# Performance work log

Hardware: AMD Instinct MI355X
Metric: run time of the kernel (lower is better)

Reference implementation:

```python
import jax, jax.numpy as jnp
import numpy as np

B, D, H = 64, 2048, 2048


def setup_inputs() -> dict:
    key = jax.random.key(0)
    ks = jax.random.split(key, 10)
    s = 1.0 / np.sqrt(D)  # Linear init scale
    # small z scale keeps exp() gates in a sane range
    return {
        "t": jnp.zeros((), jnp.float32),
        "z": jax.random.normal(ks[0], (B, D), jnp.float32) * 0.02,
        "K": jax.random.normal(ks[1], (B, D), jnp.float32) * 0.02,
        "V": jax.random.normal(ks[2], (B, D, D), jnp.float32) * 0.02,
        "Wq": jax.random.normal(ks[3], (D, D), jnp.float32) * s,
        "bq": jnp.zeros((D,), jnp.float32),
        "Wk": jax.random.normal(ks[4], (D, D), jnp.float32) * s,
        "bk": jnp.zeros((D,), jnp.float32),
        "Wv": jax.random.normal(ks[5], (D, D), jnp.float32) * s,
        "bv": jnp.zeros((D,), jnp.float32),
        "W1": jax.random.normal(ks[6], (D, H), jnp.float32) * s,
        "b1": jnp.zeros((H,), jnp.float32),
        "W2": jax.random.normal(ks[7], (H, D), jnp.float32) * (1.0 / np.sqrt(H)),
        "b2": jnp.zeros((D,), jnp.float32),
    }


def reference(t, z, K, V, Wq, bq, Wk, bk, Wv, bv, W1, b1, W2, b2):
    # get_ode_gradient_nn: 2-layer tanh MLP (stand-in for user ode_func_net)
    dz = jnp.tanh(z @ W1 + b1) @ W2 + b2                 # [B, D]
    dK = jnp.exp(z @ Wk + bk)                            # exp gate, [B, D]
    v = z @ Wv + bv                                      # [B, D]
    dV = jnp.einsum("bd,be->bde", v, dK)                # rank-1 outer update, [B, D, D]
    q = jnp.exp(z @ Wq + bq)                             # [B, D]
    a = jnp.sum(q * dK, axis=-1, keepdims=True)          # q . dK, [B, 1]
    dq = q * (dz @ Wq + bq)                              # [B, D]
    da = a + jnp.sum(dq * K, axis=-1, keepdims=True)     # [B, 1]
    dc = jnp.einsum("bde,be->bd", dV, q) + jnp.einsum("bde,be->bd", V, dq)  # [B, D]
    return (dz, da, dc, dK, dV)
```

## Files before the change

kernel.cpp:

```cpp
#include <hip/hip_runtime.h>
#include <cstddef>
#include <math.h>

#define BB 64
#define DD 2048
#define HH 2048
#define BD (BB*DD)
#define WN (2048*2048)

typedef unsigned short u16;
typedef __attribute__((ext_vector_type(8))) short bf16x8;
typedef __attribute__((ext_vector_type(4))) float f32x4;
typedef __attribute__((ext_vector_type(4))) float f4;

__device__ __forceinline__ u16 f2b(float x) {
    union { float f; unsigned u; } v; v.f = x;
    unsigned r = v.u + 0x7FFFu + ((v.u >> 16) & 1u);
    return (u16)(r >> 16);
}

__device__ __forceinline__ void gload16(const void* g, void* l) {
    __builtin_amdgcn_global_load_lds(
        (__attribute__((address_space(1))) void*)g,
        (__attribute__((address_space(3))) void*)l, 16, 0, 0);
}


__device__ __forceinline__ void wconv_tile(
    u16* sm, const float* __restrict__ W, u16* __restrict__ T,
    int kb, int nb)
{
    int t = threadIdx.x;
    int k0 = kb * 64, n0 = nb * 64;
    {
        int r = t >> 2, c0 = (t & 3) * 16;
        const float* src = W + (size_t)(k0 + r) * DD + n0 + c0;
#pragma unroll
        for (int q = 0; q < 4; ++q) {
            float4 f = *(const float4*)(src + q * 4);
            sm[r * 66 + c0 + q*4 + 0] = f2b(f.x);
            sm[r * 66 + c0 + q*4 + 1] = f2b(f.y);
            sm[r * 66 + c0 + q*4 + 2] = f2b(f.z);
            sm[r * 66 + c0 + q*4 + 3] = f2b(f.w);
        }
    }
    __syncthreads();
    {
        int rn = t >> 2, ck = (t & 3) * 16;
        u16 o[16];
#pragma unroll
        for (int j = 0; j < 16; ++j) o[j] = sm[(ck + j) * 66 + rn];
        u16* dst = T + (size_t)(n0 + rn) * DD + k0 + ck;
        *(bf16x8*)dst       = *(bf16x8*)&o[0];
        *(bf16x8*)(dst + 8) = *(bf16x8*)&o[8];
    }
}

template<int NS>
__device__ __forceinline__ void gemm_fullk(
    u16* sm, const u16* __restrict__ A0, const u16* __restrict__ A1,
    const u16* __restrict__ Wt, int nblk, f32x4* acc0, f32x4* acc1)
{
    constexpr int NS1 = NS + 1;
    constexpr int REG = NS1 * 2048;
    const int t = threadIdx.x, w = t >> 6, lane = t & 63;
    const int n0 = nblk * 64;
    const int srow = lane >> 2;
    const int sk   = (lane & 3) * 8;

    const u16* gA0 = A0 + (size_t)(w * 16 + srow) * DD + sk;
    const u16* gA1 = (NS == 2) ? A1 + (size_t)(w * 16 + srow) * DD + sk : A0;
    const u16* gW  = Wt + (size_t)(n0 + w * 16 + srow) * DD + sk;
    const int woff = w * 512;

    const int lane15 = lane & 15;
    const int k8 = (lane >> 4) * 8;

    auto stage = [&](int it, int buf) {
        u16* base = sm + buf * REG;
        gload16(gA0 + it * 32, base + woff);
        if constexpr (NS == 2) gload16(gA1 + it * 32, base + 2048 + woff);
        gload16(gW + it * 32, base + (NS1 - 1) * 2048 + woff);
    };

    constexpr int nt = DD / 32;
    stage(0, 0);
    stage(1, 1);
    for (int it = 0; it < nt; ++it) {
        const int cur = it % 3;
        if (it + 2 < nt) {
            stage(it + 2, (it + 2) % 3);
            if constexpr (NS == 1) asm volatile("s_waitcnt vmcnt(4)" ::: "memory");
            else                   asm volatile("s_waitcnt vmcnt(6)" ::: "memory");
        } else if (it + 1 < nt) {
            if constexpr (NS == 1) asm volatile("s_waitcnt vmcnt(2)" ::: "memory");
            else                   asm volatile("s_waitcnt vmcnt(3)" ::: "memory");
        } else {
            asm volatile("s_waitcnt vmcnt(0)" ::: "memory");
        }
        __builtin_amdgcn_s_barrier();

        const u16* base = sm + cur * REG;
        bf16x8 bfrag = *(const bf16x8*)&base[(NS1-1)*2048 + (w*16 + lane15)*32 + k8];
#pragma unroll
        for (int mt = 0; mt < 4; ++mt) {
            bf16x8 a0 = *(const bf16x8*)&base[(mt*16 + lane15)*32 + k8];
            acc0[mt] = __builtin_amdgcn_mfma_f32_16x16x32_bf16(a0, bfrag, acc0[mt], 0, 0, 0);
        }
        if constexpr (NS == 2) {
#pragma unroll
            for (int mt = 0; mt < 4; ++mt) {
                bf16x8 a1 = *(const bf16x8*)&base[2048 + (mt*16 + lane15)*32 + k8];
                acc1[mt] = __builtin_amdgcn_mfma_f32_16x16x32_bf16(a1, bfrag, acc1[mt], 0, 0, 0);
            }
        }
        __builtin_amdgcn_s_barrier();
    }
}

__device__ __forceinline__ void dv_body(
    const float* __restrict__ v, const float* __restrict__ dK,
    float* __restrict__ dV, int b, int chunk)
{
    int wave = threadIdx.x >> 6;
    int lane = threadIdx.x & 63;

    const f4* dK4 = (const f4*)(dK + ((size_t)b << 11));
    f4 dKr[8];
#pragma unroll
    for (int u = 0; u < 8; ++u) dKr[u] = dK4[u * 64 + lane];

    int row0 = chunk * 64 + wave * 16;
    for (int rr = 0; rr < 16; ++rr) {
        int row = row0 + rr;
        float vr = v[((size_t)b << 11) + row];
        f4* dV4 = (f4*)(dV + (((size_t)((b << 11) | row)) << 11));
#pragma unroll
        for (int u = 0; u < 8; ++u) {
            f4 o = vr * dKr[u];
            __builtin_nontemporal_store(o, &dV4[u * 64 + lane]);
        }
    }
}


__global__ __launch_bounds__(256) void wconv1(
    const float* __restrict__ W1, const float* __restrict__ Wk,
    const float* __restrict__ Wv, u16* __restrict__ W1t,
    u16* __restrict__ Wkt, u16* __restrict__ Wvt,
    const float* __restrict__ z, u16* __restrict__ zb)
{
    __shared__ u16 sm[64 * 66];
    int t = threadIdx.x;
    if (blockIdx.z == 3) {
        if (blockIdx.y != 0 || blockIdx.x >= 32) return;
        int i0 = blockIdx.x * 4096 + t * 16;
        u16 o[16];
#pragma unroll
        for (int q = 0; q < 4; ++q) {
            float4 f = *(const float4*)&z[i0 + q * 4];
            o[q*4+0] = f2b(f.x); o[q*4+1] = f2b(f.y);
            o[q*4+2] = f2b(f.z); o[q*4+3] = f2b(f.w);
        }
        *(bf16x8*)&zb[i0]     = *(bf16x8*)&o[0];
        *(bf16x8*)&zb[i0 + 8] = *(bf16x8*)&o[8];
        return;
    }
    const float* W = (blockIdx.z == 0) ? W1 : (blockIdx.z == 1) ? Wk : Wv;
    u16* T = (blockIdx.z == 0) ? W1t : (blockIdx.z == 1) ? Wkt : Wvt;
    wconv_tile(sm, W, T, blockIdx.x, blockIdx.y);
}

__global__ __launch_bounds__(256) void mA(
    const u16* __restrict__ zb, const u16* __restrict__ W1t,
    const u16* __restrict__ Wkt, const u16* __restrict__ Wvt,
    const float* __restrict__ b1, const float* __restrict__ bk,
    const float* __restrict__ bv, u16* __restrict__ hb,
    float* __restrict__ dKo, float* __restrict__ vo,
    const float* __restrict__ W2, const float* __restrict__ Wq,
    u16* __restrict__ W2t, u16* __restrict__ Wqt)
{
    __shared__ u16 sm[3 * 4096];
    int blk = blockIdx.x;
    if (blk < 96) {
        int sel  = blk >> 5;
        int nblk = blk & 31;
        const u16* Wt = (sel == 0) ? W1t : (sel == 1) ? Wkt : Wvt;
        f32x4 acc[4];
#pragma unroll
        for (int mt = 0; mt < 4; ++mt) acc[mt] = (f32x4){0.f,0.f,0.f,0.f};
        gemm_fullk<1>(sm, zb, zb, Wt, nblk, acc, nullptr);

        int w = threadIdx.x >> 6, lane = threadIdx.x & 63;
        int col = nblk * 64 + w * 16 + (lane & 15);
        int r4  = (lane >> 4) * 4;
        if (sel == 0) {
            float bb = b1[col];
#pragma unroll
            for (int mt = 0; mt < 4; ++mt)
#pragma unroll
                for (int j = 0; j < 4; ++j)
                    hb[(size_t)(mt*16 + r4 + j) * DD + col] =
                        f2b(tanhf(acc[mt][j] + bb));
        } else if (sel == 1) {
            float bb = bk[col];
#pragma unroll
            for (int mt = 0; mt < 4; ++mt)
#pragma unroll
                for (int j = 0; j < 4; ++j)
                    dKo[(size_t)(mt*16 + r4 + j) * DD + col] =
                        expf(acc[mt][j] + bb);
        } else {
            float bb = bv[col];
#pragma unroll
            for (int mt = 0; mt < 4; ++mt)
#pragma unroll
                for (int j = 0; j < 4; ++j)
                    vo[(size_t)(mt*16 + r4 + j) * DD + col] =
                        acc[mt][j] + bb;
        }
    } else {
        int r = blk - 96;
        const float* W = (r < 1024) ? W2 : Wq;
        u16* T         = (r < 1024) ? W2t : Wqt;
        int rr = r & 1023;
        wconv_tile(sm, W, T, rr & 31, rr >> 5);
    }
}

__global__ __launch_bounds__(256) void mDZ(
    const u16* __restrict__ hb, const u16* __restrict__ W2t,
    const float* __restrict__ b2, float* __restrict__ dz,
    u16* __restrict__ dzb,
    const float* __restrict__ v, const float* __restrict__ dK,
    float* __restrict__ dV)
{
    __shared__ u16 sm[3 * 4096];
    int blk = blockIdx.x;
    if (blk < 32) {
        f32x4 acc[4];
#pragma unroll
        for (int mt = 0; mt < 4; ++mt) acc[mt] = (f32x4){0.f,0.f,0.f,0.f};
        gemm_fullk<1>(sm, hb, hb, W2t, blk, acc, nullptr);

        int w = threadIdx.x >> 6, lane = threadIdx.x & 63;
        int col = blk * 64 + w * 16 + (lane & 15);
        int r4  = (lane >> 4) * 4;
        float bb = b2[col];
#pragma unroll
        for (int mt = 0; mt < 4; ++mt)
#pragma unroll
            for (int j = 0; j < 4; ++j) {
                float s = acc[mt][j] + bb;
                size_t idx = (size_t)(mt*16 + r4 + j) * DD + col;
                dz[idx]  = s;
                dzb[idx] = f2b(s);
            }
    } else {
        int r = blk - 32;
        dv_body(v, dK, dV, r >> 5, r & 31);
    }
}

__global__ __launch_bounds__(256) void mQ(
    const u16* __restrict__ zb, const u16* __restrict__ dzb,
    const u16* __restrict__ Wqt, const float* __restrict__ bq,
    float* __restrict__ qo, float* __restrict__ dqo,
    const float* __restrict__ v, const float* __restrict__ dK,
    float* __restrict__ dV)
{
    __shared__ u16 sm[3 * 6144];
    int blk = blockIdx.x;
    if (blk < 32) {
        f32x4 az[4], ad[4];
#pragma unroll
        for (int mt = 0; mt < 4; ++mt) {
            az[mt] = (f32x4){0.f,0.f,0.f,0.f};
            ad[mt] = (f32x4){0.f,0.f,0.f,0.f};
        }
        gemm_fullk<2>(sm, zb, dzb, Wqt, blk, az, ad);

        int w = threadIdx.x >> 6, lane = threadIdx.x & 63;
        int col = blk * 64 + w * 16 + (lane & 15);
        int r4  = (lane >> 4) * 4;
        float bb = bq[col];
#pragma unroll
        for (int mt = 0; mt < 4; ++mt)
#pragma unroll
            for (int j = 0; j < 4; ++j) {
                float qv = expf(az[mt][j] + bb);
                size_t idx = (size_t)(mt*16 + r4 + j) * DD + col;
                qo[idx]  = qv;
                dqo[idx] = qv * (ad[mt][j] + bb);
            }
    } else {
        int r = blk - 32;
        dv_body(v, dK, dV, 32 + (r >> 5), r & 31);
    }
}

__global__ __launch_bounds__(256) void reduce_a_da(
    const float* __restrict__ q, const float* __restrict__ dK,
    const float* __restrict__ dq, const float* __restrict__ Kin,
    float* __restrict__ a_ws, float* __restrict__ da_out)
{
    int b = blockIdx.x;
    int t = threadIdx.x;
    const float* qb  = q   + (size_t)b * DD;
    const float* dKb = dK  + (size_t)b * DD;
    const float* dqb = dq  + (size_t)b * DD;
    const float* Kb  = Kin + (size_t)b * DD;

    float s1 = 0.f, s2 = 0.f;
    for (int i = t; i < DD; i += 256) {
        s1 = fmaf(qb[i],  dKb[i], s1);
        s2 = fmaf(dqb[i], Kb[i],  s2);
    }
#pragma unroll
    for (int off = 32; off; off >>= 1) {
        s1 += __shfl_down(s1, off);
        s2 += __shfl_down(s2, off);
    }
    __shared__ float r1[4], r2[4];
    if ((t & 63) == 0) { r1[t >> 6] = s1; r2[t >> 6] = s2; }
    __syncthreads();
    if (t == 0) {
        float a  = r1[0] + r1[1] + r1[2] + r1[3];
        float k2 = r2[0] + r2[1] + r2[2] + r2[3];
        a_ws[b]   = a;
        da_out[b] = a + k2;
    }
}

__global__ __launch_bounds__(256) void dc_dot(
    const float* __restrict__ V, const float* __restrict__ v,
    const float* __restrict__ dq, const float* __restrict__ a,
    float* __restrict__ dc)
{
    int b     = blockIdx.x >> 5;
    int chunk = blockIdx.x & 31;
    int wave  = threadIdx.x >> 6;
    int lane  = threadIdx.x & 63;

    const f4* dq4 = (const f4*)(dq + ((size_t)b << 11));
    f4 dqr[8];
#pragma unroll
    for (int u = 0; u < 8; ++u) dqr[u] = dq4[u * 64 + lane];
    float ab = a[b];

    int row0 = chunk * 64 + wave * 16;
    for (int g = 0; g < 4; ++g) {
        float dot[4];
#pragma unroll
        for (int r2i = 0; r2i < 4; ++r2i) {
            int row = row0 + g * 4 + r2i;
            const f4* V4 = (const f4*)(V + (((size_t)((b << 11) | row)) << 11));
            float d = 0.f;
#pragma unroll
            for (int u = 0; u < 8; ++u) {
                f4 Vv = __builtin_nontemporal_load(&V4[u * 64 + lane]);
                d += Vv[0] * dqr[u][0] + Vv[1] * dqr[u][1]
                   + Vv[2] * dqr[u][2] + Vv[3] * dqr[u][3];
            }
            dot[r2i] = d;
        }
#pragma unroll
        for (int r2i = 0; r2i < 4; ++r2i) {
            float d = dot[r2i];
#pragma unroll
            for (int s = 32; s; s >>= 1) d += __shfl_down(d, s);
            if (lane == 0) {
                int row = row0 + g * 4 + r2i;
                dc[((size_t)b << 11) + row] =
                    v[((size_t)b << 11) + row] * ab + d;
            }
        }
    }
}

template<int MT>
__device__ __forceinline__ void gemm_body_f32(
    const float* __restrict__ A0, const float* __restrict__ A1,
    const float* __restrict__ W, float* __restrict__ part, int kc)
{
    constexpr int KC = 32;
    constexpr int RT = MT / 16;
    __shared__ float As[KC][MT];
    __shared__ float Ws[KC][64];

    const int t  = threadIdx.x;
    const int n0 = blockIdx.x * 64;
    const int k0 = blockIdx.y * kc;
    const int i  = t >> 4;
    const int j  = t & 15;

    float acc[RT][4];
#pragma unroll
    for (int r = 0; r < RT; ++r)
#pragma unroll
        for (int c = 0; c < 4; ++c) acc[r][c] = 0.f;

    for (int kk0 = 0; kk0 < kc; kk0 += KC) {
        {
            int kk = t >> 3;
            int nn = (t & 7) << 3;
            const float* s = W + (size_t)(k0 + kk0 + kk) * DD + n0 + nn;
            *(float4*)&Ws[kk][nn]     = *(const float4*)s;
            *(float4*)&Ws[kk][nn + 4] = *(const float4*)(s + 4);
        }
        if constexpr (MT == 64) {
            int m  = t & 63;
            int kb = (t >> 6) << 3;
            const float* s = A0 + (size_t)m * DD + k0 + kk0 + kb;
            float4 a0 = *(const float4*)s;
            float4 a1 = *(const float4*)(s + 4);
            As[kb+0][m] = a0.x; As[kb+1][m] = a0.y;
            As[kb+2][m] = a0.z; As[kb+3][m] = a0.w;
            As[kb+4][m] = a1.x; As[kb+5][m] = a1.y;
            As[kb+6][m] = a1.z; As[kb+7][m] = a1.w;
        } else {
            int m  = t & 127;
            int kb = (t >> 7) << 4;
            const float* base = (m < 64) ? (A0 + (size_t)m * DD)
                                         : (A1 + (size_t)(m - 64) * DD);
            const float* s = base + k0 + kk0 + kb;
#pragma unroll
            for (int p = 0; p < 4; ++p) {
                float4 av = *(const float4*)(s + p * 4);
                As[kb+p*4+0][m] = av.x; As[kb+p*4+1][m] = av.y;
                As[kb+p*4+2][m] = av.z; As[kb+p*4+3][m] = av.w;
            }
        }
        __syncthreads();
#pragma unroll
        for (int kk = 0; kk < KC; ++kk) {
            float4 wv = *(float4*)&Ws[kk][j << 2];
#pragma unroll
            for (int rq = 0; rq < RT / 4; ++rq) {
                float4 av = *(float4*)&As[kk][i * RT + rq * 4];
                acc[rq*4+0][0] = fmaf(av.x, wv.x, acc[rq*4+0][0]);
                acc[rq*4+0][1] = fmaf(av.x, wv.y, acc[rq*4+0][1]);
                acc[rq*4+0][2] = fmaf(av.x, wv.z, acc[rq*4+0][2]);
                acc[rq*4+0][3] = fmaf(av.x, wv.w, acc[rq*4+0][3]);
                acc[rq*4+1][0] = fmaf(av.y, wv.x, acc[rq*4+1][0]);
                acc[rq*4+1][1] = fmaf(av.y, wv.y, acc[rq*4+1][1]);
                acc[rq*4+1][2] = fmaf(av.y, wv.z, acc[rq*4+1][2]);
                acc[rq*4+1][3] = fmaf(av.y, wv.w, acc[rq*4+1][3]);
                acc[rq*4+2][0] = fmaf(av.z, wv.x, acc[rq*4+2][0]);
                acc[rq*4+2][1] = fmaf(av.z, wv.y, acc[rq*4+2][1]);
                acc[rq*4+2][2] = fmaf(av.z, wv.z, acc[rq*4+2][2]);
                acc[rq*4+2][3] = fmaf(av.z, wv.w, acc[rq*4+2][3]);
                acc[rq*4+3][0] = fmaf(av.w, wv.x, acc[rq*4+3][0]);
                acc[rq*4+3][1] = fmaf(av.w, wv.y, acc[rq*4+3][1]);
                acc[rq*4+3][2] = fmaf(av.w, wv.z, acc[rq*4+3][2]);
                acc[rq*4+3][3] = fmaf(av.w, wv.w, acc[rq*4+3][3]);
            }
        }
        __syncthreads();
    }

    float* P = part + (size_t)blockIdx.y * MT * DD + n0 + (j << 2);
#pragma unroll
    for (int r = 0; r < RT; ++r)
        *(float4*)&P[(size_t)(i * RT + r) * DD] =
            make_float4(acc[r][0], acc[r][1], acc[r][2], acc[r][3]);
}

__global__ __launch_bounds__(256) void gemm64(
    const float* __restrict__ A, const float* __restrict__ W,
    float* __restrict__ part, int kc)
{ gemm_body_f32<64>(A, A, W, part, kc); }

__global__ __launch_bounds__(256) void gemm64_z2(
    const float* __restrict__ A,
    const float* __restrict__ W0, const float* __restrict__ W1,
    float* __restrict__ p0, float* __restrict__ p1, int kc)
{
    const float* W = blockIdx.z ? W1 : W0;
    float*       P = blockIdx.z ? p1 : p0;
    gemm_body_f32<64>(A, A, W, P, kc);
}

__global__ __launch_bounds__(256) void gemm128(
    const float* __restrict__ A0, const float* __restrict__ A1,
    const float* __restrict__ W, float* __restrict__ part, int kc)
{ gemm_body_f32<128>(A0, A1, W, part, kc); }

__global__ __launch_bounds__(256) void epilogue_f32(
    const float* __restrict__ part, const float* __restrict__ bias,
    float* __restrict__ out, int act, int KS)
{
    int i = blockIdx.x * 256 + threadIdx.x;
    float s = bias[i & (DD - 1)];
    for (int ks = 0; ks < KS; ++ks) s += part[(size_t)ks * BD + i];
    if (act == 1) s = tanhf(s);
    out[i] = s;
}

__global__ __launch_bounds__(256) void ep_kv_f32(
    const float* __restrict__ pk, const float* __restrict__ pv,
    const float* __restrict__ bk, const float* __restrict__ bv,
    float* __restrict__ dKo, float* __restrict__ vo, int KS)
{
    int i = blockIdx.x * 256 + threadIdx.x;
    int d = i & (DD - 1);
    float sk = 0.f, sv = 0.f;
    for (int ks = 0; ks < KS; ++ks) {
        sk += pk[(size_t)ks * BD + i];
        sv += pv[(size_t)ks * BD + i];
    }
    dKo[i] = expf(sk + bk[d]);
    vo[i]  = sv + bv[d];
}

__global__ __launch_bounds__(256) void ep_q_dq_f32(
    const float* __restrict__ pq, const float* __restrict__ bq,
    float* __restrict__ qo, float* __restrict__ dqo, int KS)
{
    int i = blockIdx.x * 256 + threadIdx.x;
    int b = i >> 11, d = i & (DD - 1);
    float sq = 0.f, sd = 0.f;
    for (int ks = 0; ks < KS; ++ks) {
        const float* P = pq + (size_t)ks * (128 * DD);
        sq += P[(size_t)b * DD + d];
        sd += P[(size_t)(b + 64) * DD + d];
    }
    float bb = bq[d];
    float qv = expf(sq + bb);
    qo[i]  = qv;
    dqo[i] = qv * (sd + bb);
}

__global__ __launch_bounds__(256) void dv_write_full(
    const float* __restrict__ v, const float* __restrict__ dK,
    float* __restrict__ dV)
{
    dv_body(v, dK, dV, blockIdx.x >> 5, blockIdx.x & 31);
}

extern "C" void kernel_launch(void* const* d_in, const int* in_sizes, int n_in,
                              void* d_out, int out_size, void* d_ws, size_t ws_size,
                              hipStream_t stream)
{
    const float* z   = (const float*)d_in[1];
    const float* Kin = (const float*)d_in[2];
    const float* Vin = (const float*)d_in[3];
    const float* Wq  = (const float*)d_in[4];
    const float* bq  = (const float*)d_in[5];
    const float* Wk  = (const float*)d_in[6];
    const float* bk  = (const float*)d_in[7];
    const float* Wv  = (const float*)d_in[8];
    const float* bv  = (const float*)d_in[9];
    const float* W1  = (const float*)d_in[10];
    const float* b1  = (const float*)d_in[11];
    const float* W2  = (const float*)d_in[12];
    const float* b2  = (const float*)d_in[13];

    float* out   = (float*)d_out;
    float* o_dz  = out;
    float* o_da  = out + BD;
    float* o_dc  = out + BD + BB;
    float* o_dK  = out + 2 * BD + BB;
    float* o_dV  = out + 3 * BD + BB;

    float* ws    = (float*)d_ws;
    float* ws_v  = ws;
    float* ws_q  = ws + BD;
    float* ws_dq = ws + 2 * BD;
    float* ws_a  = ws + 3 * BD;
    float* ws_h  = ws + 3 * BD + 64;
    u16*   zb    = (u16*)(ws + 4 * BD + 64);
    u16*   hb    = zb + BD;
    u16*   dzb   = hb + BD;
    u16*   wt    = dzb + BD;

    const size_t pre_fl = 4ull * BD + 64 + (3ull * BD + 5ull * WN) / 2;

    dim3 blk(256);

    if (pre_fl * 4ull <= ws_size) {
        u16* W1t = wt;
        u16* W2t = wt + 1ull * WN;
        u16* Wkt = wt + 2ull * WN;
        u16* Wvt = wt + 3ull * WN;
        u16* Wqt = wt + 4ull * WN;

        wconv1<<<dim3(32, 32, 4), blk, 0, stream>>>(
            W1, Wk, Wv, W1t, Wkt, Wvt, z, zb);

        mA<<<dim3(96 + 2048), blk, 0, stream>>>(
            zb, W1t, Wkt, Wvt, b1, bk, bv, hb, o_dK, ws_v, W2, Wq, W2t, Wqt);

        mDZ<<<dim3(32 + 1024), blk, 0, stream>>>(
            hb, W2t, b2, o_dz, dzb, ws_v, o_dK, o_dV);

        mQ<<<dim3(32 + 1024), blk, 0, stream>>>(
            zb, dzb, Wqt, bq, ws_q, ws_dq, ws_v, o_dK, o_dV);
    } else {
        float* pool = ws + 4 * BD + 64;
        int KSf = 16;
        while (KSf > 1 &&
               ((size_t)(4 * BD + 64) + 2ull * KSf * BD) * 4ull > ws_size)
            KSf >>= 1;
        int kc = DD / KSf;
        float* p0 = pool;
        float* p1 = pool + (size_t)KSf * BD;

        dim3 gG(DD / 64, KSf);
        dim3 gG2(DD / 64, KSf, 2);
        dim3 gE(BD / 256);

        gemm64<<<gG, blk, 0, stream>>>(z, W1, p0, kc);
        epilogue_f32<<<gE, blk, 0, stream>>>(p0, b1, ws_h, 1, KSf);

        gemm64<<<gG, blk, 0, stream>>>(ws_h, W2, p0, kc);
        epilogue_f32<<<gE, blk, 0, stream>>>(p0, b2, o_dz, 0, KSf);

        gemm64_z2<<<gG2, blk, 0, stream>>>(z, Wk, Wv, p0, p1, kc);
        ep_kv_f32<<<gE, blk, 0, stream>>>(p0, p1, bk, bv, o_dK, ws_v, KSf);

        dv_write_full<<<dim3(BB * 32), blk, 0, stream>>>(ws_v, o_dK, o_dV);

        gemm128<<<gG, blk, 0, stream>>>(z, o_dz, Wq, p0, kc);
        ep_q_dq_f32<<<gE, blk, 0, stream>>>(p0, bq, ws_q, ws_dq, KSf);
    }

    reduce_a_da<<<dim3(BB), blk, 0, stream>>>(ws_q, o_dK, ws_dq, Kin, ws_a, o_da);

    dc_dot<<<dim3(BB * 32), blk, 0, stream>>>(Vin, ws_v, ws_dq, ws_a, o_dc);
}
```

Baseline: 411.5 us.

## Fuse fp32 weight conversion into GEMM staging, dropping pre-transposed bf16 weight copies

```diff
diff --git a/kernel.cpp b/kernel.cpp
--- a/kernel.cpp
+++ b/kernel.cpp
@@ -6,7 +6,6 @@
 #define DD 2048
 #define HH 2048
 #define BD (BB*DD)
-#define WN (2048*2048)
 
 typedef unsigned short u16;
 typedef __attribute__((ext_vector_type(8))) short bf16x8;
@@ -19,102 +18,89 @@
     return (u16)(r >> 16);
 }
 
-__device__ __forceinline__ void gload16(const void* g, void* l) {
-    __builtin_amdgcn_global_load_lds(
-        (__attribute__((address_space(1))) void*)g,
-        (__attribute__((address_space(3))) void*)l, 16, 0, 0);
-}
-
-
-__device__ __forceinline__ void wconv_tile(
-    u16* sm, const float* __restrict__ W, u16* __restrict__ T,
-    int kb, int nb)
-{
-    int t = threadIdx.x;
-    int k0 = kb * 64, n0 = nb * 64;
-    {
-        int r = t >> 2, c0 = (t & 3) * 16;
-        const float* src = W + (size_t)(k0 + r) * DD + n0 + c0;
-#pragma unroll
-        for (int q = 0; q < 4; ++q) {
-            float4 f = *(const float4*)(src + q * 4);
-            sm[r * 66 + c0 + q*4 + 0] = f2b(f.x);
-            sm[r * 66 + c0 + q*4 + 1] = f2b(f.y);
-            sm[r * 66 + c0 + q*4 + 2] = f2b(f.z);
-            sm[r * 66 + c0 + q*4 + 3] = f2b(f.w);
-        }
-    }
-    __syncthreads();
-    {
-        int rn = t >> 2, ck = (t & 3) * 16;
-        u16 o[16];
-#pragma unroll
-        for (int j = 0; j < 16; ++j) o[j] = sm[(ck + j) * 66 + rn];
-        u16* dst = T + (size_t)(n0 + rn) * DD + k0 + ck;
-        *(bf16x8*)dst       = *(bf16x8*)&o[0];
-        *(bf16x8*)(dst + 8) = *(bf16x8*)&o[8];
-    }
-}
-
 template<int NS>
-__device__ __forceinline__ void gemm_fullk(
+__device__ __forceinline__ void gemm_fk2(
     u16* sm, const u16* __restrict__ A0, const u16* __restrict__ A1,
-    const u16* __restrict__ Wt, int nblk, f32x4* acc0, f32x4* acc1)
+    const float* __restrict__ W, int nblk, f32x4* acc0, f32x4* acc1)
 {
     constexpr int NS1 = NS + 1;
     constexpr int REG = NS1 * 2048;
     const int t = threadIdx.x, w = t >> 6, lane = t & 63;
     const int n0 = nblk * 64;
-    const int srow = lane >> 2;
-    const int sk   = (lane & 3) * 8;
-
-    const u16* gA0 = A0 + (size_t)(w * 16 + srow) * DD + sk;
-    const u16* gA1 = (NS == 2) ? A1 + (size_t)(w * 16 + srow) * DD + sk : A0;
-    const u16* gW  = Wt + (size_t)(n0 + w * 16 + srow) * DD + sk;
-    const int woff = w * 512;
-
+
+    const int am  = t >> 2;
+    const int ak8 = (t & 3) * 8;
+    const int kp = t >> 4;
+    const int c4 = (t & 15) * 4;
     const int lane15 = lane & 15;
-    const int k8 = (lane >> 4) * 8;
-
-    auto stage = [&](int it, int buf) {
-        u16* base = sm + buf * REG;
-        gload16(gA0 + it * 32, base + woff);
-        if constexpr (NS == 2) gload16(gA1 + it * 32, base + 2048 + woff);
-        gload16(gW + it * 32, base + (NS1 - 1) * 2048 + woff);
+    const int k8f = (lane >> 4) * 8;
+
+    const u16* pa0 = A0 + (size_t)am * DD + ak8;
+    const u16* pa1 = (NS == 2) ? A1 + (size_t)am * DD + ak8 : pa0;
+    const float* pw = W + (size_t)(2 * kp) * DD + n0 + c4;
+
+    struct R { bf16x8 a0; bf16x8 a1; float4 w0, w1; };
+    R Ra, Rb;
+
+    auto issue = [&](int it, R& r) {
+        r.a0 = *(const bf16x8*)(pa0 + it * 32);
+        if constexpr (NS == 2) r.a1 = *(const bf16x8*)(pa1 + it * 32);
+        r.w0 = *(const float4*)(pw + (size_t)it * 32 * DD);
+        r.w1 = *(const float4*)(pw + (size_t)it * 32 * DD + DD);
     };
-
-    constexpr int nt = DD / 32;
-    stage(0, 0);
-    stage(1, 1);
-    for (int it = 0; it < nt; ++it) {
-        const int cur = it % 3;
-        if (it + 2 < nt) {
-            stage(it + 2, (it + 2) % 3);
-            if constexpr (NS == 1) asm volatile("s_waitcnt vmcnt(4)" ::: "memory");
-            else                   asm volatile("s_waitcnt vmcnt(6)" ::: "memory");
-        } else if (it + 1 < nt) {
-            if constexpr (NS == 1) asm volatile("s_waitcnt vmcnt(2)" ::: "memory");
-            else                   asm volatile("s_waitcnt vmcnt(3)" ::: "memory");
-        } else {
-            asm volatile("s_waitcnt vmcnt(0)" ::: "memory");
-        }
+    auto store = [&](R& r, u16* buf) {
+        *(bf16x8*)(buf + am * 32 + ak8) = r.a0;
+        if constexpr (NS == 2)
+            *(bf16x8*)(buf + 2048 + am * 32 + ak8) = r.a1;
+        u16* wb = buf + (NS1 - 1) * 2048;
+        unsigned p;
+        p = (unsigned)f2b(r.w0.x) | ((unsigned)f2b(r.w1.x) << 16);
+        *(unsigned*)(wb + (c4 + 0) * 32 + 2 * kp) = p;
+        p = (unsigned)f2b(r.w0.y) | ((unsigned)f2b(r.w1.y) << 16);
+        *(unsigned*)(wb + (c4 + 1) * 32 + 2 * kp) = p;
+        p = (unsigned)f2b(r.w0.z) | ((unsigned)f2b(r.w1.z) << 16);
+        *(unsigned*)(wb + (c4 + 2) * 32 + 2 * kp) = p;
+        p = (unsigned)f2b(r.w0.w) | ((unsigned)f2b(r.w1.w) << 16);
+        *(unsigned*)(wb + (c4 + 3) * 32 + 2 * kp) = p;
+    };
+    auto compute = [&](const u16* buf) {
+        bf16x8 bfrag = *(const bf16x8*)(buf + (NS1 - 1) * 2048
+                                        + (w * 16 + lane15) * 32 + k8f);
+#pragma unroll
+        for (int mt = 0; mt < 4; ++mt) {
+            bf16x8 a = *(const bf16x8*)(buf + (mt * 16 + lane15) * 32 + k8f);
+            acc0[mt] = __builtin_amdgcn_mfma_f32_16x16x32_bf16(
+                a, bfrag, acc0[mt], 0, 0, 0);
+        }
+        if constexpr (NS == 2) {
+#pragma unroll
+            for (int mt = 0; mt < 4; ++mt) {
+                bf16x8 a = *(const bf16x8*)(buf + 2048
+                                            + (mt * 16 + lane15) * 32 + k8f);
+                acc1[mt] = __builtin_amdgcn_mfma_f32_16x16x32_bf16(
+                    a, bfrag, acc1[mt], 0, 0, 0);
+            }
+        }
+    };
+
+    u16* b0 = sm;
+    u16* b1 = sm + REG;
+    issue(0, Ra);
+    issue(1, Rb);
+#pragma unroll 1
+    for (int it2 = 0; it2 < 32; ++it2) {
+        store(Ra, b0);
+        if (it2 < 31) issue(2 * it2 + 2, Ra);
+        asm volatile("s_waitcnt lgkmcnt(0)" ::: "memory");
         __builtin_amdgcn_s_barrier();
-
-        const u16* base = sm + cur * REG;
-        bf16x8 bfrag = *(const bf16x8*)&base[(NS1-1)*2048 + (w*16 + lane15)*32 + k8];
-#pragma unroll
-        for (int mt = 0; mt < 4; ++mt) {
-            bf16x8 a0 = *(const bf16x8*)&base[(mt*16 + lane15)*32 + k8];
-            acc0[mt] = __builtin_amdgcn_mfma_f32_16x16x32_bf16(a0, bfrag, acc0[mt], 0, 0, 0);
-        }
-        if constexpr (NS == 2) {
-#pragma unroll
-            for (int mt = 0; mt < 4; ++mt) {
-                bf16x8 a1 = *(const bf16x8*)&base[2048 + (mt*16 + lane15)*32 + k8];
-                acc1[mt] = __builtin_amdgcn_mfma_f32_16x16x32_bf16(a1, bfrag, acc1[mt], 0, 0, 0);
-            }
-        }
+        __builtin_amdgcn_sched_barrier(0);
+        compute(b0);
+        store(Rb, b1);
+        if (it2 < 31) issue(2 * it2 + 3, Rb);
+        asm volatile("s_waitcnt lgkmcnt(0)" ::: "memory");
         __builtin_amdgcn_s_barrier();
+        __builtin_amdgcn_sched_barrier(0);
+        compute(b1);
     }
 }
 
@@ -144,104 +130,78 @@
 }
 
 
-__global__ __launch_bounds__(256) void wconv1(
-    const float* __restrict__ W1, const float* __restrict__ Wk,
-    const float* __restrict__ Wv, u16* __restrict__ W1t,
-    u16* __restrict__ Wkt, u16* __restrict__ Wvt,
+__global__ __launch_bounds__(256) void zconv(
     const float* __restrict__ z, u16* __restrict__ zb)
 {
-    __shared__ u16 sm[64 * 66];
-    int t = threadIdx.x;
-    if (blockIdx.z == 3) {
-        if (blockIdx.y != 0 || blockIdx.x >= 32) return;
-        int i0 = blockIdx.x * 4096 + t * 16;
-        u16 o[16];
-#pragma unroll
-        for (int q = 0; q < 4; ++q) {
-            float4 f = *(const float4*)&z[i0 + q * 4];
-            o[q*4+0] = f2b(f.x); o[q*4+1] = f2b(f.y);
-            o[q*4+2] = f2b(f.z); o[q*4+3] = f2b(f.w);
-        }
-        *(bf16x8*)&zb[i0]     = *(bf16x8*)&o[0];
-        *(bf16x8*)&zb[i0 + 8] = *(bf16x8*)&o[8];
-        return;
-    }
-    const float* W = (blockIdx.z == 0) ? W1 : (blockIdx.z == 1) ? Wk : Wv;
-    u16* T = (blockIdx.z == 0) ? W1t : (blockIdx.z == 1) ? Wkt : Wvt;
-    wconv_tile(sm, W, T, blockIdx.x, blockIdx.y);
+    int i = (blockIdx.x * 256 + threadIdx.x) * 4;
+    float4 f = *(const float4*)&z[i];
+    union { u16 u[4]; uint2 v; } o;
+    o.u[0] = f2b(f.x); o.u[1] = f2b(f.y); o.u[2] = f2b(f.z); o.u[3] = f2b(f.w);
+    *(uint2*)&zb[i] = o.v;
 }
 
 __global__ __launch_bounds__(256) void mA(
-    const u16* __restrict__ zb, const u16* __restrict__ W1t,
-    const u16* __restrict__ Wkt, const u16* __restrict__ Wvt,
+    const u16* __restrict__ zb, const float* __restrict__ W1,
+    const float* __restrict__ Wk, const float* __restrict__ Wv,
     const float* __restrict__ b1, const float* __restrict__ bk,
     const float* __restrict__ bv, u16* __restrict__ hb,
-    float* __restrict__ dKo, float* __restrict__ vo,
-    const float* __restrict__ W2, const float* __restrict__ Wq,
-    u16* __restrict__ W2t, u16* __restrict__ Wqt)
-{
-    __shared__ u16 sm[3 * 4096];
+    float* __restrict__ dKo, float* __restrict__ vo)
+{
+    __shared__ u16 sm[2 * 2 * 2048];
     int blk = blockIdx.x;
-    if (blk < 96) {
-        int sel  = blk >> 5;
-        int nblk = blk & 31;
-        const u16* Wt = (sel == 0) ? W1t : (sel == 1) ? Wkt : Wvt;
-        f32x4 acc[4];
-#pragma unroll
-        for (int mt = 0; mt < 4; ++mt) acc[mt] = (f32x4){0.f,0.f,0.f,0.f};
-        gemm_fullk<1>(sm, zb, zb, Wt, nblk, acc, nullptr);
-
-        int w = threadIdx.x >> 6, lane = threadIdx.x & 63;
-        int col = nblk * 64 + w * 16 + (lane & 15);
-        int r4  = (lane >> 4) * 4;
-        if (sel == 0) {
-            float bb = b1[col];
-#pragma unroll
-            for (int mt = 0; mt < 4; ++mt)
-#pragma unroll
-                for (int j = 0; j < 4; ++j)
-                    hb[(size_t)(mt*16 + r4 + j) * DD + col] =
-                        f2b(tanhf(acc[mt][j] + bb));
-        } else if (sel == 1) {
-            float bb = bk[col];
-#pragma unroll
-            for (int mt = 0; mt < 4; ++mt)
-#pragma unroll
-                for (int j = 0; j < 4; ++j)
-                    dKo[(size_t)(mt*16 + r4 + j) * DD + col] =
-                        expf(acc[mt][j] + bb);
-        } else {
-            float bb = bv[col];
-#pragma unroll
-            for (int mt = 0; mt < 4; ++mt)
-#pragma unroll
-                for (int j = 0; j < 4; ++j)
-                    vo[(size_t)(mt*16 + r4 + j) * DD + col] =
-                        acc[mt][j] + bb;
-        }
+    int sel  = blk >> 5;
+    int nblk = blk & 31;
+    const float* W = (sel == 0) ? W1 : (sel == 1) ? Wk : Wv;
+
+    f32x4 acc[4];
+#pragma unroll
+    for (int mt = 0; mt < 4; ++mt) acc[mt] = (f32x4){0.f, 0.f, 0.f, 0.f};
+    gemm_fk2<1>(sm, zb, zb, W, nblk, acc, nullptr);
+
+    int w = threadIdx.x >> 6, lane = threadIdx.x & 63;
+    int col = nblk * 64 + w * 16 + (lane & 15);
+    int r4  = (lane >> 4) * 4;
+    if (sel == 0) {
+        float bb = b1[col];
+#pragma unroll
+        for (int mt = 0; mt < 4; ++mt)
+#pragma unroll
+            for (int j = 0; j < 4; ++j)
+                hb[(size_t)(mt * 16 + r4 + j) * DD + col] =
+                    f2b(tanhf(acc[mt][j] + bb));
+    } else if (sel == 1) {
+        float bb = bk[col];
+#pragma unroll
+        for (int mt = 0; mt < 4; ++mt)
+#pragma unroll
+            for (int j = 0; j < 4; ++j)
+                dKo[(size_t)(mt * 16 + r4 + j) * DD + col] =
+                    expf(acc[mt][j] + bb);
     } else {
-        int r = blk - 96;
-        const float* W = (r < 1024) ? W2 : Wq;
-        u16* T         = (r < 1024) ? W2t : Wqt;
-        int rr = r & 1023;
-        wconv_tile(sm, W, T, rr & 31, rr >> 5);
+        float bb = bv[col];
+#pragma unroll
+        for (int mt = 0; mt < 4; ++mt)
+#pragma unroll
+            for (int j = 0; j < 4; ++j)
+                vo[(size_t)(mt * 16 + r4 + j) * DD + col] =
+                    acc[mt][j] + bb;
     }
 }
 
 __global__ __launch_bounds__(256) void mDZ(
-    const u16* __restrict__ hb, const u16* __restrict__ W2t,
+    const u16* __restrict__ hb, const float* __restrict__ W2,
     const float* __restrict__ b2, float* __restrict__ dz,
     u16* __restrict__ dzb,
     const float* __restrict__ v, const float* __restrict__ dK,
     float* __restrict__ dV)
 {
-    __shared__ u16 sm[3 * 4096];
+    __shared__ u16 sm[2 * 2 * 2048];
     int blk = blockIdx.x;
     if (blk < 32) {
         f32x4 acc[4];
 #pragma unroll
-        for (int mt = 0; mt < 4; ++mt) acc[mt] = (f32x4){0.f,0.f,0.f,0.f};
-        gemm_fullk<1>(sm, hb, hb, W2t, blk, acc, nullptr);
+        for (int mt = 0; mt < 4; ++mt) acc[mt] = (f32x4){0.f, 0.f, 0.f, 0.f};
+        gemm_fk2<1>(sm, hb, hb, W2, blk, acc, nullptr);
 
         int w = threadIdx.x >> 6, lane = threadIdx.x & 63;
         int col = blk * 64 + w * 16 + (lane & 15);
@@ -252,7 +212,7 @@
 #pragma unroll
             for (int j = 0; j < 4; ++j) {
                 float s = acc[mt][j] + bb;
-                size_t idx = (size_t)(mt*16 + r4 + j) * DD + col;
+                size_t idx = (size_t)(mt * 16 + r4 + j) * DD + col;
                 dz[idx]  = s;
                 dzb[idx] = f2b(s);
             }
@@ -264,21 +224,21 @@
 
 __global__ __launch_bounds__(256) void mQ(
     const u16* __restrict__ zb, const u16* __restrict__ dzb,
-    const u16* __restrict__ Wqt, const float* __restrict__ bq,
+    const float* __restrict__ Wq, const float* __restrict__ bq,
     float* __restrict__ qo, float* __restrict__ dqo,
     const float* __restrict__ v, const float* __restrict__ dK,
     float* __restrict__ dV)
 {
-    __shared__ u16 sm[3 * 6144];
+    __shared__ u16 sm[2 * 3 * 2048];
     int blk = blockIdx.x;
     if (blk < 32) {
         f32x4 az[4], ad[4];
 #pragma unroll
         for (int mt = 0; mt < 4; ++mt) {
-            az[mt] = (f32x4){0.f,0.f,0.f,0.f};
-            ad[mt] = (f32x4){0.f,0.f,0.f,0.f};
-        }
-        gemm_fullk<2>(sm, zb, dzb, Wqt, blk, az, ad);
+            az[mt] = (f32x4){0.f, 0.f, 0.f, 0.f};
+            ad[mt] = (f32x4){0.f, 0.f, 0.f, 0.f};
+        }
+        gemm_fk2<2>(sm, zb, dzb, Wq, blk, az, ad);
 
         int w = threadIdx.x >> 6, lane = threadIdx.x & 63;
         int col = blk * 64 + w * 16 + (lane & 15);
@@ -289,7 +249,7 @@
 #pragma unroll
             for (int j = 0; j < 4; ++j) {
                 float qv = expf(az[mt][j] + bb);
-                size_t idx = (size_t)(mt*16 + r4 + j) * DD + col;
+                size_t idx = (size_t)(mt * 16 + r4 + j) * DD + col;
                 qo[idx]  = qv;
                 dqo[idx] = qv * (ad[mt][j] + bb);
             }
@@ -572,30 +532,22 @@
     u16*   zb    = (u16*)(ws + 4 * BD + 64);
     u16*   hb    = zb + BD;
     u16*   dzb   = hb + BD;
-    u16*   wt    = dzb + BD;
-
-    const size_t pre_fl = 4ull * BD + 64 + (3ull * BD + 5ull * WN) / 2;
+
+    const size_t pre_fl = 4ull * BD + 64 + (3ull * BD + 1) / 2;
 
     dim3 blk(256);
 
     if (pre_fl * 4ull <= ws_size) {
-        u16* W1t = wt;
-        u16* W2t = wt + 1ull * WN;
-        u16* Wkt = wt + 2ull * WN;
-        u16* Wvt = wt + 3ull * WN;
-        u16* Wqt = wt + 4ull * WN;
-
-        wconv1<<<dim3(32, 32, 4), blk, 0, stream>>>(
-            W1, Wk, Wv, W1t, Wkt, Wvt, z, zb);
-
-        mA<<<dim3(96 + 2048), blk, 0, stream>>>(
-            zb, W1t, Wkt, Wvt, b1, bk, bv, hb, o_dK, ws_v, W2, Wq, W2t, Wqt);
+        zconv<<<dim3(BD / 1024), blk, 0, stream>>>(z, zb);
+
+        mA<<<dim3(96), blk, 0, stream>>>(
+            zb, W1, Wk, Wv, b1, bk, bv, hb, o_dK, ws_v);
 
         mDZ<<<dim3(32 + 1024), blk, 0, stream>>>(
-            hb, W2t, b2, o_dz, dzb, ws_v, o_dK, o_dV);
+            hb, W2, b2, o_dz, dzb, ws_v, o_dK, o_dV);
 
         mQ<<<dim3(32 + 1024), blk, 0, stream>>>(
-            zb, dzb, Wqt, bq, ws_q, ws_dq, ws_v, o_dK, o_dV);
+            zb, dzb, Wq, bq, ws_q, ws_dq, ws_v, o_dK, o_dV);
     } else {
         float* pool = ws + 4 * BD + 64;
         int KSf = 16;
```

Result: slower. 431.3 us (+4.8%).
